# Performance work log

Measured on AMD Instinct MI355X. Metric: run time of the kernel, lower is better.

Reference implementation:

```python
import jax, jax.numpy as jnp
import numpy as np

B, NF, V, D, ND = 4096, 26, 100000, 64, 13
KERNELS = (7, 5, 3)
TOPKS = (23, 8, 3)  # k-max schedule derived from n=26, l=3 per CCPM formula
BN_EPS = 1e-5


def setup_inputs() -> dict:
    key = jax.random.key(0)
    ks = jax.random.split(key, 16)
    sparse = jax.random.randint(ks[0], (B, NF), 0, V)
    dense = jax.random.normal(ks[1], (B, ND), dtype=jnp.float32)
    embed_tables = jax.random.normal(ks[2], (NF, V, D), dtype=jnp.float32) * 0.01
    # conv weights OIHW, kernel (k,1)
    cw1 = jax.random.normal(ks[3], (64, 1, 7, 1), dtype=jnp.float32) * 0.1
    cb1 = jnp.zeros((64,), jnp.float32)
    cw2 = jax.random.normal(ks[4], (32, 64, 5, 1), dtype=jnp.float32) * 0.05
    cb2 = jnp.zeros((32,), jnp.float32)
    cw3 = jax.random.normal(ks[5], (16, 32, 3, 1), dtype=jnp.float32) * 0.05
    cb3 = jnp.zeros((16,), jnp.float32)
    DIN = TOPKS[-1] * 16 * D + ND  # 3*16*64+13 = 3085
    W1 = jax.random.normal(ks[6], (DIN, 256), dtype=jnp.float32) * 0.02
    b1 = jnp.zeros((256,), jnp.float32)
    g1 = jnp.ones((256,), jnp.float32)
    be1 = jnp.zeros((256,), jnp.float32)
    W2 = jax.random.normal(ks[7], (256, 128), dtype=jnp.float32) * 0.05
    b2 = jnp.zeros((128,), jnp.float32)
    g2 = jnp.ones((128,), jnp.float32)
    be2 = jnp.zeros((128,), jnp.float32)
    W3 = jax.random.normal(ks[8], (128, 1), dtype=jnp.float32) * 0.05
    b3 = jnp.zeros((1,), jnp.float32)
    return dict(sparse=sparse, dense=dense, embed_tables=embed_tables,
                cw1=cw1, cb1=cb1, cw2=cw2, cb2=cb2, cw3=cw3, cb3=cb3,
                W1=W1, b1=b1, g1=g1, be1=be1, W2=W2, b2=b2, g2=g2, be2=be2,
                W3=W3, b3=b3)


def _cnn_layer(x, w, b, k, topk):
    # ZeroPad2d pads H (feat axis) symmetrically by k//2, nothing along W.
    y = jax.lax.conv_general_dilated(
        x, w, window_strides=(1, 1), padding=[(k // 2, k // 2), (0, 0)],
        dimension_numbers=("NCHW", "OIHW", "NCHW"))
    y = jnp.tanh(y + b[None, :, None, None])
    # torch.topk along dim=2 (H), sorted descending values
    yt = jnp.swapaxes(y, 2, 3)            # [B,C,W,H]
    vals, _ = jax.lax.top_k(yt, topk)     # [B,C,W,k]
    return jnp.swapaxes(vals, 2, 3)       # [B,C,k,W]


def _bn(x, g, b):
    mu = x.mean(0)
    var = x.var(0)
    return g * (x - mu) * jax.lax.rsqrt(var + BN_EPS) + b


def reference(sparse, dense, embed_tables, cw1, cb1, cw2, cb2, cw3, cb3,
              W1, b1, g1, be1, W2, b2, g2, be2, W3, b3):
    # sparse embedding lookup per field: [B, NF, D]
    emb = embed_tables[jnp.arange(NF)[None, :], sparse]
    x = emb[:, None, :, :]  # [B,1,NF,D]
    x = _cnn_layer(x, cw1, cb1, KERNELS[0], TOPKS[0])
    x = _cnn_layer(x, cw2, cb2, KERNELS[1], TOPKS[1])
    x = _cnn_layer(x, cw3, cb3, KERNELS[2], TOPKS[2])  # [B,16,3,64]
    flat = x.reshape(x.shape[0], -1)
    h = jnp.concatenate([flat, dense], axis=1)  # [B, 3085]
    h = jnp.tanh(_bn(h @ W1 + b1, g1, be1))
    h = jnp.tanh(_bn(h @ W2 + b2, g2, be2))
    out = (h @ W3 + b3)[:, 0]  # logits, sigmoid_out=False
    return out
```

## Files before the change

kernel.cpp:

```cpp
#include <hip/hip_runtime.h>
#include <cstdint>
#include <cstddef>

#define B_SZ   4096
#define NF     26
#define VOC    100000
#define LDH    3088
#define DIN    3085

typedef __attribute__((ext_vector_type(8))) short short8;
typedef __attribute__((ext_vector_type(4))) float f32x4;

__device__ __forceinline__ float fast_tanh(float x) {
    float e = __expf(2.0f * x);
    return 1.0f - 2.0f * __builtin_amdgcn_rcpf(e + 1.0f);
}
__device__ __forceinline__ unsigned short f2bf(float x) {
    union { float f; unsigned u; } v; v.f = x;
    return (unsigned short)((v.u + 0x7FFFu + ((v.u >> 16) & 1u)) >> 16);
}
__device__ __forceinline__ float bf2f(unsigned short u) {
    union { unsigned u; float f; } v; v.u = ((unsigned)u) << 16; return v.f;
}

template<int N>
__device__ __forceinline__ void bitonic_asc(float (&a)[N]) {
#pragma unroll
    for (int k = 2; k <= N; k <<= 1) {
#pragma unroll
        for (int j = k >> 1; j > 0; j >>= 1) {
#pragma unroll
            for (int i = 0; i < N; ++i) {
                int l = i ^ j;
                if (l > i) {
                    bool up = ((i & k) == 0);
                    float x = a[i], y = a[l];
                    float mn = fminf(x, y), mx = fmaxf(x, y);
                    a[i] = up ? mn : mx;
                    a[l] = up ? mx : mn;
                }
            }
        }
    }
}

__global__ void prep_kernel(const float* __restrict__ cw1, const float* __restrict__ cw2,
                            const float* __restrict__ cw3, const float* __restrict__ dense,
                            float* __restrict__ w1t, unsigned short* __restrict__ w2b,
                            unsigned short* __restrict__ w3b, float* __restrict__ sums,
                            float* __restrict__ hmat)
{
    int idx = blockIdx.x * blockDim.x + threadIdx.x;
    if (idx < 448) {
        int c = idx / 7, j = idx % 7;
        w1t[j * 64 + c] = cw1[idx];
    } else if (idx < 10688) {
        int o = idx - 448;
        int c2 = o / 320, k = o % 320;
        int j = k >> 6, c = k & 63;
        w2b[o] = f2bf(cw2[(c2 * 64 + c) * 5 + j]);
    } else if (idx < 12224) {
        int o = idx - 10688;
        int c3 = o / 96, k = o % 96;
        int j = k >> 5, cc = k & 31;
        w3b[o] = f2bf(cw3[(c3 * 32 + cc) * 3 + j]);
    } else if (idx < 12992) {
        sums[idx - 12224] = 0.f;
    }
    int di = idx - 12992;
    if (di >= 0 && di < B_SZ * 13) {
        int b = di / 13, j = di % 13;
        hmat[(size_t)b * LDH + 3072 + j] = dense[di];
    }
}

__global__ __launch_bounds__(256, 3) void cnn_kernel(
    const int* __restrict__ sparse, const float* __restrict__ tables,
    const float* __restrict__ w1t, const float* __restrict__ cb1,
    const unsigned short* __restrict__ w2b, const float* __restrict__ cb2,
    const unsigned short* __restrict__ w3b, const float* __restrict__ cb3,
    float* __restrict__ hmat)
{
    const int d0 = blockIdx.x * 8;
    const int b  = blockIdx.y;
    const int tid = threadIdx.x;

    __shared__ __align__(16) unsigned short t1s[8 * 1800];
    __shared__ __align__(16) unsigned short y2s[8 * 32 * 25];
    __shared__ __align__(16) unsigned short t2bf[8 * 328];
    __shared__ __align__(16) float h0s[8 * 32];
    __shared__ __align__(16) float y3s[8 * 128];
    __shared__ int sidx[NF];

    if (tid < NF) sidx[tid] = sparse[b * NF + tid];
    __syncthreads();

    for (int x = tid; x < 2560; x += 256) {
        int dd = x / 320, r = x % 320;
        int i5 = r >> 6, c = r & 63;
        int i = (i5 < 2) ? i5 : (23 + i5);
        t1s[dd * 1800 + i * 64 + c] = 0;
    }
    for (int x = tid; x < 512; x += 256) {
        int dd = x >> 6, r = x & 63;
        int i = (r >> 5) * 9, cc = r & 31;
        t2bf[dd * 328 + i * 32 + cc] = 0;
    }
    if (tid < 48) {
        int dd = tid / 6, r = tid % 6;
        int i = (r < 3) ? r : (26 + r);
        h0s[dd * 32 + i] = 0.f;
    } else {
        int t = tid - 48;
        if (t < 208) {
            int fi = t >> 3, dd = t & 7;
            h0s[dd * 32 + 3 + fi] =
                tables[((size_t)fi * VOC + sidx[fi]) * 64 + d0 + dd];
        }
    }
    __syncthreads();

#pragma unroll
    for (int t = 0; t < 2; ++t) {
        int task = tid + 256 * t;
        int dd = task >> 6, c = task & 63;
        float w1r[7];
#pragma unroll
        for (int j = 0; j < 7; ++j) w1r[j] = w1t[j * 64 + c];
        float bias = cb1[c];
        float hr[32];
#pragma unroll
        for (int i = 0; i < 32; ++i) hr[i] = h0s[dd * 32 + i];
        float arr[32];
#pragma unroll
        for (int f = 0; f < 26; ++f) {
            float s = bias;
#pragma unroll
            for (int j = 0; j < 7; ++j) s += w1r[j] * hr[f + j];
            arr[f] = fast_tanh(s);
        }
#pragma unroll
        for (int f = 26; f < 32; ++f) arr[f] = -2.0f;
        bitonic_asc<32>(arr);
        unsigned short* row = &t1s[dd * 1800 + c];
#pragma unroll
        for (int r = 0; r < 23; ++r) row[(2 + r) * 64] = f2bf(arr[31 - r]);
    }
    __syncthreads();

    {
        const int lane = tid & 63;
        const int w = tid >> 6;
        const int quad = lane >> 4;
        const int m = lane & 15;
        const int e = m >> 3, dd = m & 7;
        const int n = lane & 15;

        short8 Bf0[10], Bf1[10];
#pragma unroll
        for (int ks = 0; ks < 10; ++ks) {
            Bf0[ks] = *reinterpret_cast<const short8*>(w2b + (n * 320 + ks * 32 + quad * 8));
            Bf1[ks] = *reinterpret_cast<const short8*>(w2b + ((16 + n) * 320 + ks * 32 + quad * 8));
        }
        float bias0 = cb2[n], bias1 = cb2[16 + n];

#pragma unroll
        for (int pi = 0; pi < 3; ++pi) {
            int p = w + pi * 4;
            int f0 = 2 * p;
            f32x4 acc0 = {bias0, bias0, bias0, bias0};
            f32x4 acc1 = {bias1, bias1, bias1, bias1};
            const unsigned short* abase = &t1s[dd * 1800 + (f0 + e) * 64 + quad * 8];
#pragma unroll
            for (int ks = 0; ks < 10; ++ks) {
                short8 af = *reinterpret_cast<const short8*>(abase + ks * 32);
                acc0 = __builtin_amdgcn_mfma_f32_16x16x32_bf16(af, Bf0[ks], acc0, 0, 0, 0);
                acc1 = __builtin_amdgcn_mfma_f32_16x16x32_bf16(af, Bf1[ks], acc1, 0, 0, 0);
            }
#pragma unroll
            for (int r = 0; r < 4; ++r) {
                int mm = quad * 4 + r;
                int ee = mm >> 3, dw = mm & 7;
                int f = f0 + ee;
                if (f < 23) {
                    y2s[(dw * 32 + n) * 25 + f]      = f2bf(fast_tanh(acc0[r]));
                    y2s[(dw * 32 + 16 + n) * 25 + f] = f2bf(fast_tanh(acc1[r]));
                }
            }
        }
    }
    __syncthreads();

    {
        int dd = tid >> 5, c2 = tid & 31;
        float a[32];
        const unsigned short* src = &y2s[(dd * 32 + c2) * 25];
#pragma unroll
        for (int f = 0; f < 23; ++f) a[f] = bf2f(src[f]);
#pragma unroll
        for (int f = 23; f < 32; ++f) a[f] = -2.0f;
        bitonic_asc<32>(a);
        unsigned short* row = &t2bf[dd * 328 + c2];
#pragma unroll
        for (int r = 0; r < 8; ++r) row[(1 + r) * 32] = f2bf(a[31 - r]);
    }
    __syncthreads();

    {
        const int lane = tid & 63;
        const int w = tid >> 6;
        const int quad = lane >> 4;
        const int m = lane & 15;
        const int e = m >> 3, dd = m & 7;
        const int n = lane & 15;
        int f0 = 2 * w;

        f32x4 acc;
        float bias = cb3[n];
        acc[0] = bias; acc[1] = bias; acc[2] = bias; acc[3] = bias;
        const unsigned short* abase = &t2bf[dd * 328 + (f0 + e) * 32 + quad * 8];
#pragma unroll
        for (int ks = 0; ks < 3; ++ks) {
            short8 af = *reinterpret_cast<const short8*>(abase + ks * 32);
            short8 bf = *reinterpret_cast<const short8*>(w3b + (n * 96 + ks * 32 + quad * 8));
            acc = __builtin_amdgcn_mfma_f32_16x16x32_bf16(af, bf, acc, 0, 0, 0);
        }
#pragma unroll
        for (int r = 0; r < 4; ++r) {
            int mm = quad * 4 + r;
            int ee = mm >> 3, dw = mm & 7;
            int f = f0 + ee;
            y3s[dw * 128 + n * 8 + f] = fast_tanh(acc[r]);
        }
    }
    __syncthreads();

    if (tid < 128) {
        int dd = tid >> 4, c3 = tid & 15;
        float a[8];
#pragma unroll
        for (int f = 0; f < 8; ++f) a[f] = y3s[dd * 128 + c3 * 8 + f];
        bitonic_asc<8>(a);
        float* orow = &hmat[(size_t)b * LDH + c3 * 192 + d0 + dd];
        orow[0]   = a[7];
        orow[64]  = a[6];
        orow[128] = a[5];
    }
}

template<bool APPLY>
__global__ __launch_bounds__(256) void gemm_kernel(
    const float* __restrict__ A, int lda, int K,
    const float* __restrict__ Bm, int ldb,
    const float* __restrict__ scl, const float* __restrict__ sft,
    float* __restrict__ C, int N)
{
    __shared__ __align__(16) float As[16 * 68];
    __shared__ __align__(16) float Bs[16 * 68];
    const int tid = threadIdx.x;
    const int row0 = blockIdx.y * 64;
    const int n0 = blockIdx.x * 64;
    const int ty = tid >> 4, tx = tid & 15;

    float acc[4][4];
#pragma unroll
    for (int i = 0; i < 4; ++i)
#pragma unroll
        for (int j = 0; j < 4; ++j) acc[i][j] = 0.f;

    const int kk_a = tid & 15, rb_a = tid >> 4;
    const int kr_b = tid >> 4, nb_b = (tid & 15) * 4;

    for (int k0 = 0; k0 < K; k0 += 16) {
        __syncthreads();
        {
            int k = k0 + kk_a;
            bool ok = (k < K);
            float sc = 0.f, sh = 0.f;
            if (APPLY && ok) { sc = scl[k]; sh = sft[k]; }
#pragma unroll
            for (int p = 0; p < 4; ++p) {
                int r = rb_a + p * 16;
                float v = 0.f;
                if (ok) {
                    v = A[(size_t)(row0 + r) * lda + k];
                    if (APPLY) v = fast_tanh(v * sc + sh);
                }
                As[kk_a * 68 + r] = v;
            }
        }
        {
            int k = k0 + kr_b;
            float4 bv = make_float4(0.f, 0.f, 0.f, 0.f);
            if (k < K) bv = *reinterpret_cast<const float4*>(&Bm[(size_t)k * ldb + n0 + nb_b]);
            *reinterpret_cast<float4*>(&Bs[kr_b * 68 + nb_b]) = bv;
        }
        __syncthreads();
#pragma unroll
        for (int kk = 0; kk < 16; ++kk) {
            float4 av = *reinterpret_cast<const float4*>(&As[kk * 68 + ty * 4]);
            float4 bv = *reinterpret_cast<const float4*>(&Bs[kk * 68 + tx * 4]);
            float aa[4] = {av.x, av.y, av.z, av.w};
            float bb[4] = {bv.x, bv.y, bv.z, bv.w};
#pragma unroll
            for (int i = 0; i < 4; ++i)
#pragma unroll
                for (int j = 0; j < 4; ++j) acc[i][j] += aa[i] * bb[j];
        }
    }

#pragma unroll
    for (int i = 0; i < 4; ++i) {
        float4 ov = make_float4(acc[i][0], acc[i][1], acc[i][2], acc[i][3]);
        *reinterpret_cast<float4*>(&C[(size_t)(row0 + ty * 4 + i) * N + n0 + tx * 4]) = ov;
    }
}

__global__ void bnstats_kernel(const float* __restrict__ z, int ncols,
                               float* __restrict__ sums, float* __restrict__ sumsq)
{
    int col = threadIdx.x;
    int r0 = blockIdx.x * 256;
    float s = 0.f, q = 0.f;
    for (int i = 0; i < 256; ++i) {
        float v = z[(size_t)(r0 + i) * ncols + col];
        s += v; q += v * v;
    }
    atomicAdd(&sums[col], s);
    atomicAdd(&sumsq[col], q);
}

__global__ void bnfin_kernel(const float* __restrict__ sums, const float* __restrict__ sumsq,
                             const float* __restrict__ g, const float* __restrict__ be,
                             int ncols, float* __restrict__ scl, float* __restrict__ sft)
{
    int i = threadIdx.x + blockIdx.x * blockDim.x;
    if (i < ncols) {
        float mu = sums[i] * (1.0f / 4096.0f);
        float var = sumsq[i] * (1.0f / 4096.0f) - mu * mu;
        float s = g[i] * rsqrtf(var + 1e-5f);
        scl[i] = s;
        sft[i] = be[i] - mu * s;
    }
}

__global__ __launch_bounds__(256) void final_kernel(
    const float* __restrict__ z2, const float* __restrict__ scl, const float* __restrict__ sft,
    const float* __restrict__ W3, const float* __restrict__ b3, float* __restrict__ out)
{
    int lane = threadIdx.x & 63;
    int wv = threadIdx.x >> 6;
    int r = blockIdx.x * 4 + wv;
    float p = 0.f;
#pragma unroll
    for (int t = 0; t < 2; ++t) {
        int n = lane + t * 64;
        p += fast_tanh(z2[(size_t)r * 128 + n] * scl[n] + sft[n]) * W3[n];
    }
#pragma unroll
    for (int off = 32; off > 0; off >>= 1) p += __shfl_down(p, off);
    if (lane == 0) out[r] = p + b3[0];
}

extern "C" void kernel_launch(void* const* d_in, const int* in_sizes, int n_in,
                              void* d_out, int out_size, void* d_ws, size_t ws_size,
                              hipStream_t stream) {
    const int*   sparse = (const int*)  d_in[0];
    const float* dense  = (const float*)d_in[1];
    const float* tables = (const float*)d_in[2];
    const float* cw1    = (const float*)d_in[3];
    const float* cb1    = (const float*)d_in[4];
    const float* cw2    = (const float*)d_in[5];
    const float* cb2    = (const float*)d_in[6];
    const float* cw3    = (const float*)d_in[7];
    const float* cb3    = (const float*)d_in[8];
    const float* W1     = (const float*)d_in[9];
    const float* g1     = (const float*)d_in[11];
    const float* be1    = (const float*)d_in[12];
    const float* W2     = (const float*)d_in[13];
    const float* g2     = (const float*)d_in[15];
    const float* be2    = (const float*)d_in[16];
    const float* W3     = (const float*)d_in[17];
    const float* b3     = (const float*)d_in[18];
    float* out = (float*)d_out;

    float* ws   = (float*)d_ws;
    float* hmat = ws;
    float* z1   = hmat + (size_t)B_SZ * LDH;
    float* z2   = z1 + (size_t)B_SZ * 256;
    float* w1t  = z2 + (size_t)B_SZ * 128;
    unsigned short* w2b = (unsigned short*)(w1t + 448);
    unsigned short* w3b = (unsigned short*)(w1t + 448 + 5120);
    float* sums = w1t + 448 + 5120 + 768;
    float* a1   = sums + 768;
    float* c1   = a1 + 256;
    float* a2   = c1 + 256;
    float* c2v  = a2 + 128;

    prep_kernel<<<259, 256, 0, stream>>>(cw1, cw2, cw3, dense, w1t, w2b, w3b, sums, hmat);

    cnn_kernel<<<dim3(8, B_SZ), 256, 0, stream>>>(sparse, tables, w1t, cb1,
                                                  w2b, cb2, w3b, cb3, hmat);

    gemm_kernel<false><<<dim3(4, 64), 256, 0, stream>>>(hmat, LDH, DIN, W1, 256,
                                                        nullptr, nullptr, z1, 256);
    bnstats_kernel<<<16, 256, 0, stream>>>(z1, 256, sums, sums + 256);
    bnfin_kernel<<<1, 256, 0, stream>>>(sums, sums + 256, g1, be1, 256, a1, c1);

    gemm_kernel<true><<<dim3(2, 64), 256, 0, stream>>>(z1, 256, 256, W2, 128,
                                                       a1, c1, z2, 128);
    bnstats_kernel<<<16, 128, 0, stream>>>(z2, 128, sums + 512, sums + 640);
    bnfin_kernel<<<1, 128, 0, stream>>>(sums + 512, sums + 640, g2, be2, 128, a2, c2v);

    final_kernel<<<1024, 256, 0, stream>>>(z2, a2, c2v, W3, b3, out);
}
```

Measured before the change: 1.819 ms.

## Defer tanh past top-k, use odd-even merge sorts, shrink GEMM tiles, widen BN stats grid

```diff
diff --git a/kernel.cpp b/kernel.cpp
--- a/kernel.cpp
+++ b/kernel.cpp
@@ -19,26 +19,57 @@
     union { float f; unsigned u; } v; v.f = x;
     return (unsigned short)((v.u + 0x7FFFu + ((v.u >> 16) & 1u)) >> 16);
 }
-__device__ __forceinline__ float bf2f(unsigned short u) {
-    union { unsigned u; float f; } v; v.u = ((unsigned)u) << 16; return v.f;
+__device__ __forceinline__ unsigned short f2h(float x) {
+    union { _Float16 h; unsigned short u; } v; v.h = (_Float16)x; return v.u;
+}
+__device__ __forceinline__ float h2f(unsigned short u) {
+    union { unsigned short u; _Float16 h; } v; v.u = u; return (float)v.h;
 }
 
 template<int N>
-__device__ __forceinline__ void bitonic_asc(float (&a)[N]) {
-#pragma unroll
-    for (int k = 2; k <= N; k <<= 1) {
-#pragma unroll
-        for (int j = k >> 1; j > 0; j >>= 1) {
-#pragma unroll
-            for (int i = 0; i < N; ++i) {
-                int l = i ^ j;
-                if (l > i) {
-                    bool up = ((i & k) == 0);
-                    float x = a[i], y = a[l];
-                    float mn = fminf(x, y), mx = fmaxf(x, y);
-                    a[i] = up ? mn : mx;
-                    a[l] = up ? mx : mn;
+__device__ __forceinline__ void oem_sort(float (&a)[N]) {
+#pragma unroll
+    for (int p = 1; p < N; p <<= 1) {
+#pragma unroll
+        for (int k = p; k >= 1; k >>= 1) {
+#pragma unroll
+            for (int j = k % p; j + k < N; j += 2 * k) {
+#pragma unroll
+                for (int i = 0; i < k; ++i) {
+                    int lo = i + j, hi = i + j + k;
+                    if (hi < N && (lo / (2 * p) == hi / (2 * p))) {
+                        float x = a[lo], y = a[hi];
+                        a[lo] = fminf(x, y);
+                        a[hi] = fmaxf(x, y);
+                    }
                 }
+            }
+        }
+    }
+}
+
+__device__ __forceinline__ void bclean8(float (&a)[8]) {
+#pragma unroll
+    for (int j = 4; j >= 1; j >>= 1) {
+#pragma unroll
+        for (int i = 0; i < 8; ++i) {
+            if ((i & j) == 0 && (i | j) < 8) {
+                float x = a[i], y = a[i + j];
+                a[i] = fminf(x, y);
+                a[i + j] = fmaxf(x, y);
+            }
+        }
+    }
+}
+__device__ __forceinline__ void bclean4(float (&a)[4]) {
+#pragma unroll
+    for (int j = 2; j >= 1; j >>= 1) {
+#pragma unroll
+        for (int i = 0; i < 4; ++i) {
+            if ((i & j) == 0 && (i | j) < 4) {
+                float x = a[i], y = a[i + j];
+                a[i] = fminf(x, y);
+                a[i + j] = fmaxf(x, y);
             }
         }
     }
@@ -131,20 +162,18 @@
         float hr[32];
 #pragma unroll
         for (int i = 0; i < 32; ++i) hr[i] = h0s[dd * 32 + i];
-        float arr[32];
+        float arr[26];
 #pragma unroll
         for (int f = 0; f < 26; ++f) {
             float s = bias;
 #pragma unroll
             for (int j = 0; j < 7; ++j) s += w1r[j] * hr[f + j];
-            arr[f] = fast_tanh(s);
-        }
-#pragma unroll
-        for (int f = 26; f < 32; ++f) arr[f] = -2.0f;
-        bitonic_asc<32>(arr);
+            arr[f] = s;
+        }
+        oem_sort<26>(arr);
         unsigned short* row = &t1s[dd * 1800 + c];
 #pragma unroll
-        for (int r = 0; r < 23; ++r) row[(2 + r) * 64] = f2bf(arr[31 - r]);
+        for (int r = 0; r < 23; ++r) row[(2 + r) * 64] = f2bf(fast_tanh(arr[25 - r]));
     }
     __syncthreads();
 
@@ -183,8 +212,8 @@
                 int ee = mm >> 3, dw = mm & 7;
                 int f = f0 + ee;
                 if (f < 23) {
-                    y2s[(dw * 32 + n) * 25 + f]      = f2bf(fast_tanh(acc0[r]));
-                    y2s[(dw * 32 + 16 + n) * 25 + f] = f2bf(fast_tanh(acc1[r]));
+                    y2s[(dw * 32 + n) * 25 + f]      = f2h(acc0[r]);
+                    y2s[(dw * 32 + 16 + n) * 25 + f] = f2h(acc1[r]);
                 }
             }
         }
@@ -193,16 +222,29 @@
 
     {
         int dd = tid >> 5, c2 = tid & 31;
-        float a[32];
         const unsigned short* src = &y2s[(dd * 32 + c2) * 25];
-#pragma unroll
-        for (int f = 0; f < 23; ++f) a[f] = bf2f(src[f]);
-#pragma unroll
-        for (int f = 23; f < 32; ++f) a[f] = -2.0f;
-        bitonic_asc<32>(a);
+        float va[8], vb[8], vc[7];
+#pragma unroll
+        for (int f = 0; f < 8; ++f) va[f] = h2f(src[f]);
+#pragma unroll
+        for (int f = 0; f < 8; ++f) vb[f] = h2f(src[8 + f]);
+#pragma unroll
+        for (int f = 0; f < 7; ++f) vc[f] = h2f(src[16 + f]);
+        oem_sort<8>(va);
+        oem_sort<8>(vb);
+        oem_sort<7>(vc);
+        float mg[8];
+#pragma unroll
+        for (int i = 0; i < 8; ++i) mg[i] = fmaxf(va[i], vb[7 - i]);
+        bclean8(mg);
+        float m2[8];
+        m2[7] = mg[7];
+#pragma unroll
+        for (int i = 0; i < 7; ++i) m2[i] = fmaxf(mg[i], vc[6 - i]);
+        bclean8(m2);
         unsigned short* row = &t2bf[dd * 328 + c2];
 #pragma unroll
-        for (int r = 0; r < 8; ++r) row[(1 + r) * 32] = f2bf(a[31 - r]);
+        for (int r = 0; r < 8; ++r) row[(1 + r) * 32] = f2bf(fast_tanh(m2[7 - r]));
     }
     __syncthreads();
 
@@ -230,21 +272,27 @@
             int mm = quad * 4 + r;
             int ee = mm >> 3, dw = mm & 7;
             int f = f0 + ee;
-            y3s[dw * 128 + n * 8 + f] = fast_tanh(acc[r]);
+            y3s[dw * 128 + n * 8 + f] = acc[r];
         }
     }
     __syncthreads();
 
     if (tid < 128) {
         int dd = tid >> 4, c3 = tid & 15;
-        float a[8];
-#pragma unroll
-        for (int f = 0; f < 8; ++f) a[f] = y3s[dd * 128 + c3 * 8 + f];
-        bitonic_asc<8>(a);
+        const float* yb = &y3s[dd * 128 + c3 * 8];
+        float a4[4], b4[4];
+#pragma unroll
+        for (int f = 0; f < 4; ++f) { a4[f] = yb[f]; b4[f] = yb[4 + f]; }
+        oem_sort<4>(a4);
+        oem_sort<4>(b4);
+        float mg[4];
+#pragma unroll
+        for (int i = 0; i < 4; ++i) mg[i] = fmaxf(a4[i], b4[3 - i]);
+        bclean4(mg);
         float* orow = &hmat[(size_t)b * LDH + c3 * 192 + d0 + dd];
-        orow[0]   = a[7];
-        orow[64]  = a[6];
-        orow[128] = a[5];
+        orow[0]   = fast_tanh(mg[3]);
+        orow[64]  = fast_tanh(mg[2]);
+        orow[128] = fast_tanh(mg[1]);
     }
 }
 
@@ -255,16 +303,16 @@
     const float* __restrict__ scl, const float* __restrict__ sft,
     float* __restrict__ C, int N)
 {
-    __shared__ __align__(16) float As[16 * 68];
+    __shared__ __align__(16) float As[16 * 36];
     __shared__ __align__(16) float Bs[16 * 68];
     const int tid = threadIdx.x;
-    const int row0 = blockIdx.y * 64;
+    const int row0 = blockIdx.y * 32;
     const int n0 = blockIdx.x * 64;
     const int ty = tid >> 4, tx = tid & 15;
 
-    float acc[4][4];
-#pragma unroll
-    for (int i = 0; i < 4; ++i)
+    float acc[2][4];
+#pragma unroll
+    for (int i = 0; i < 2; ++i)
 #pragma unroll
         for (int j = 0; j < 4; ++j) acc[i][j] = 0.f;
 
@@ -279,14 +327,14 @@
             float sc = 0.f, sh = 0.f;
             if (APPLY && ok) { sc = scl[k]; sh = sft[k]; }
 #pragma unroll
-            for (int p = 0; p < 4; ++p) {
+            for (int p = 0; p < 2; ++p) {
                 int r = rb_a + p * 16;
                 float v = 0.f;
                 if (ok) {
                     v = A[(size_t)(row0 + r) * lda + k];
                     if (APPLY) v = fast_tanh(v * sc + sh);
                 }
-                As[kk_a * 68 + r] = v;
+                As[kk_a * 36 + r] = v;
             }
         }
         {
@@ -298,21 +346,21 @@
         __syncthreads();
 #pragma unroll
         for (int kk = 0; kk < 16; ++kk) {
-            float4 av = *reinterpret_cast<const float4*>(&As[kk * 68 + ty * 4]);
+            float2 av = *reinterpret_cast<const float2*>(&As[kk * 36 + ty * 2]);
             float4 bv = *reinterpret_cast<const float4*>(&Bs[kk * 68 + tx * 4]);
-            float aa[4] = {av.x, av.y, av.z, av.w};
             float bb[4] = {bv.x, bv.y, bv.z, bv.w};
 #pragma unroll
-            for (int i = 0; i < 4; ++i)
-#pragma unroll
-                for (int j = 0; j < 4; ++j) acc[i][j] += aa[i] * bb[j];
-        }
-    }
-
-#pragma unroll
-    for (int i = 0; i < 4; ++i) {
+            for (int j = 0; j < 4; ++j) {
+                acc[0][j] += av.x * bb[j];
+                acc[1][j] += av.y * bb[j];
+            }
+        }
+    }
+
+#pragma unroll
+    for (int i = 0; i < 2; ++i) {
         float4 ov = make_float4(acc[i][0], acc[i][1], acc[i][2], acc[i][3]);
-        *reinterpret_cast<float4*>(&C[(size_t)(row0 + ty * 4 + i) * N + n0 + tx * 4]) = ov;
+        *reinterpret_cast<float4*>(&C[(size_t)(row0 + ty * 2 + i) * N + n0 + tx * 4]) = ov;
     }
 }
 
@@ -320,9 +368,10 @@
                                float* __restrict__ sums, float* __restrict__ sumsq)
 {
     int col = threadIdx.x;
-    int r0 = blockIdx.x * 256;
+    int r0 = blockIdx.x * 16;
     float s = 0.f, q = 0.f;
-    for (int i = 0; i < 256; ++i) {
+#pragma unroll
+    for (int i = 0; i < 16; ++i) {
         float v = z[(size_t)(r0 + i) * ncols + col];
         s += v; q += v * v;
     }
@@ -402,14 +451,14 @@
     cnn_kernel<<<dim3(8, B_SZ), 256, 0, stream>>>(sparse, tables, w1t, cb1,
                                                   w2b, cb2, w3b, cb3, hmat);
 
-    gemm_kernel<false><<<dim3(4, 64), 256, 0, stream>>>(hmat, LDH, DIN, W1, 256,
-                                                        nullptr, nullptr, z1, 256);
-    bnstats_kernel<<<16, 256, 0, stream>>>(z1, 256, sums, sums + 256);
+    gemm_kernel<false><<<dim3(4, 128), 256, 0, stream>>>(hmat, LDH, DIN, W1, 256,
+                                                         nullptr, nullptr, z1, 256);
+    bnstats_kernel<<<256, 256, 0, stream>>>(z1, 256, sums, sums + 256);
     bnfin_kernel<<<1, 256, 0, stream>>>(sums, sums + 256, g1, be1, 256, a1, c1);
 
-    gemm_kernel<true><<<dim3(2, 64), 256, 0, stream>>>(z1, 256, 256, W2, 128,
-                                                       a1, c1, z2, 128);
-    bnstats_kernel<<<16, 128, 0, stream>>>(z2, 128, sums + 512, sums + 640);
+    gemm_kernel<true><<<dim3(2, 128), 256, 0, stream>>>(z1, 256, 256, W2, 128,
+                                                        a1, c1, z2, 128);
+    bnstats_kernel<<<256, 128, 0, stream>>>(z2, 128, sums + 512, sums + 640);
     bnfin_kernel<<<1, 128, 0, stream>>>(sums + 512, sums + 640, g2, be2, 128, a2, c2v);
 
     final_kernel<<<1024, 256, 0, stream>>>(z2, a2, c2v, W3, b3, out);
```

After: 1.569 ms. 13.8% less time.
